# Performance work log

Measured on AMD Instinct MI355X. Metric: run time of the kernel, lower is better.

The kernel has to match this reference:

```python
import jax, jax.numpy as jnp
import numpy as np

B, S, D = 4, 2048, 768
H = 12
DH = D // H
FF = 4 * D
EPS = 1e-5


def _layernorm(x, g, b):
    mu = jnp.mean(x, axis=-1, keepdims=True)
    var = jnp.mean(jnp.square(x - mu), axis=-1, keepdims=True)
    return (x - mu) * jax.lax.rsqrt(var + EPS) * g + b


def setup_inputs() -> dict:
    key = jax.random.key(0)
    ks = jax.random.split(key, 16)
    s_d = 1.0 / np.sqrt(D)
    s_ff = 1.0 / np.sqrt(FF)
    inp = {
        "x": jax.random.normal(ks[0], (B, S, D), jnp.float32),
        # LayerNorm 1
        "ln1_g": jnp.ones((D,), jnp.float32),
        "ln1_b": jnp.zeros((D,), jnp.float32),
        # attention linears (stored as [in, out], i.e. already transposed)
        "Wq": jax.random.normal(ks[1], (D, D), jnp.float32) * s_d,
        "bq": jax.random.normal(ks[2], (D,), jnp.float32) * s_d,
        "Wk": jax.random.normal(ks[3], (D, D), jnp.float32) * s_d,
        "bk": jax.random.normal(ks[4], (D,), jnp.float32) * s_d,
        "Wv": jax.random.normal(ks[5], (D, D), jnp.float32) * s_d,
        "bv": jax.random.normal(ks[6], (D,), jnp.float32) * s_d,
        "Wo": jax.random.normal(ks[7], (D, D), jnp.float32) * s_d,
        "bo": jax.random.normal(ks[8], (D,), jnp.float32) * s_d,
        # LayerNorm 2
        "ln2_g": jnp.ones((D,), jnp.float32),
        "ln2_b": jnp.zeros((D,), jnp.float32),
        # feed-forward (bias always on, per torch code)
        "W1": jax.random.normal(ks[9], (D, FF), jnp.float32) * s_d,
        "b1": jax.random.normal(ks[10], (FF,), jnp.float32) * s_d,
        "W2": jax.random.normal(ks[11], (FF, D), jnp.float32) * s_ff,
        "b2": jax.random.normal(ks[12], (D,), jnp.float32) * s_ff,
    }
    return inp


def reference(x, ln1_g, ln1_b, Wq, bq, Wk, bk, Wv, bv, Wo, bo,
              ln2_g, ln2_b, W1, b1, W2, b2):
    # --- attention branch (pre-LN) ---
    h = _layernorm(x, ln1_g, ln1_b)
    q = (h @ Wq + bq).reshape(B, S, H, DH).transpose(0, 2, 1, 3)  # [B,H,S,DH]
    k = (h @ Wk + bk).reshape(B, S, H, DH).transpose(0, 2, 1, 3)
    v = (h @ Wv + bv).reshape(B, S, H, DH).transpose(0, 2, 1, 3)
    scores = jnp.einsum("bhqd,bhkd->bhqk", q, k) / np.sqrt(DH)
    causal = jnp.tril(jnp.ones((S, S), bool))
    scores = jnp.where(causal, scores, -jnp.inf)
    attn = jax.nn.softmax(scores, axis=-1)
    out = jnp.einsum("bhqk,bhkd->bhqd", attn, v)
    out = out.transpose(0, 2, 1, 3).reshape(B, S, D)
    x = x + (out @ Wo + bo)
    # --- feed-forward branch (pre-LN, exact GELU) ---
    h2 = _layernorm(x, ln2_g, ln2_b)
    ff = jax.nn.gelu(h2 @ W1 + b1, approximate=False) @ W2 + b2
    return x + ff
```

## Files before the change

kernel.cpp:

```cpp
#include <hip/hip_runtime.h>
#include <math.h>

#define B_ 4
#define S_ 2048
#define D_ 768
#define H_ 12
#define DH_ 64
#define FF_ 3072
#define LDQ (3*D_)

using short8  = __attribute__((ext_vector_type(8))) short;
using f32x4   = __attribute__((ext_vector_type(4))) float;
using f32x16  = __attribute__((ext_vector_type(16))) float;
using float4v = __attribute__((ext_vector_type(4))) float;
using ushort4v= __attribute__((ext_vector_type(4))) unsigned short;

__device__ __forceinline__ unsigned short f2bf(float f) {
  unsigned u = __builtin_bit_cast(unsigned, f);
  u += 0x7FFFu + ((u >> 16) & 1u);
  return (unsigned short)(u >> 16);
}

__device__ __forceinline__ unsigned cvt_pk_bf16(float a, float b) {
  unsigned r;
  asm("v_cvt_pk_bf16_f32 %0, %1, %2" : "=v"(r) : "v"(a), "v"(b));
  return r;
}

__device__ __forceinline__ void gload16(const void* g, void* l) {
  __builtin_amdgcn_global_load_lds(
      (const __attribute__((address_space(1))) unsigned*)g,
      (__attribute__((address_space(3))) unsigned*)l, 16, 0, 0);
}

__global__ __launch_bounds__(256) void transpose_cast_multi_kernel(
    const float* __restrict__ Wq, const float* __restrict__ Wk,
    const float* __restrict__ Wv, const float* __restrict__ Wo,
    const float* __restrict__ W1, const float* __restrict__ W2,
    unsigned short* __restrict__ WqT, unsigned short* __restrict__ WkT,
    unsigned short* __restrict__ WvT, unsigned short* __restrict__ WoT,
    unsigned short* __restrict__ W1T, unsigned short* __restrict__ W2T) {
  __shared__ float tile[32][33];
  int bid = blockIdx.x;
  const float* in; unsigned short* out; int K, N, t;
  if (bid < 2304) {
    int seg = bid / 576; t = bid % 576; K = D_; N = D_;
    in  = seg == 0 ? Wq  : seg == 1 ? Wk  : seg == 2 ? Wv  : Wo;
    out = seg == 0 ? WqT : seg == 1 ? WkT : seg == 2 ? WvT : WoT;
  } else if (bid < 4608) {
    t = bid - 2304; K = D_; N = FF_; in = W1; out = W1T;
  } else {
    t = bid - 4608; K = FF_; N = D_; in = W2; out = W2T;
  }
  int ntk = K / 32;
  int k0 = (t % ntk) * 32, n0 = (t / ntk) * 32;
  int tx = threadIdx.x, ty = threadIdx.y;
#pragma unroll
  for (int i = 0; i < 4; i++)
    tile[ty + 8*i][tx] = in[(size_t)(k0 + ty + 8*i) * N + n0 + tx];
  __syncthreads();
#pragma unroll
  for (int i = 0; i < 4; i++)
    out[(size_t)(n0 + ty + 8*i) * K + k0 + tx] = f2bf(tile[tx][ty + 8*i]);
}

__global__ void bias_cat_kernel(const float* __restrict__ bq, const float* __restrict__ bk,
                                const float* __restrict__ bv, float* __restrict__ dst) {
  int i = blockIdx.x * 256 + threadIdx.x;
  if (i >= 3 * D_) return;
  float v;
  if (i < D_)            v = bq[i];
  else if (i < 2 * D_)   v = bk[i - D_];
  else                   v = bv[i - 2 * D_];
  dst[i] = v;
}

__global__ __launch_bounds__(256) void layernorm_kernel(
    const float* __restrict__ x, const float* __restrict__ g,
    const float* __restrict__ b, unsigned short* __restrict__ out) {
  int wave = threadIdx.x >> 6, lane = threadIdx.x & 63;
  int row = blockIdx.x * 4 + wave;
  const float* xr = x + (size_t)row * D_;
  float4v v[3];
  float sum = 0.f, sq = 0.f;
#pragma unroll
  for (int i = 0; i < 3; i++) {
    v[i] = reinterpret_cast<const float4v*>(xr)[lane + 64*i];
#pragma unroll
    for (int j = 0; j < 4; j++) { sum += v[i][j]; sq += v[i][j]*v[i][j]; }
  }
#pragma unroll
  for (int d = 1; d < 64; d <<= 1) { sum += __shfl_xor(sum, d); sq += __shfl_xor(sq, d); }
  float mu   = sum * (1.0f / D_);
  float var  = sq  * (1.0f / D_) - mu * mu;
  float rstd = rsqrtf(var + 1e-5f);
  unsigned short* orow = out + (size_t)row * D_;
#pragma unroll
  for (int i = 0; i < 3; i++) {
    int idx = (lane + 64*i) * 4;
    ushort4v o;
#pragma unroll
    for (int j = 0; j < 4; j++)
      o[j] = f2bf((v[i][j] - mu) * rstd * g[idx + j] + b[idx + j]);
    *reinterpret_cast<ushort4v*>(orow + idx) = o;
  }
}

#define EPI_QKV   0
#define EPI_OPROJ 1
#define EPI_GELU  2
#define EPI_FINAL 3

template<int EPI>
__global__ __launch_bounds__(256) void gemm_kernel(
    const unsigned short* __restrict__ A, int lda,
    const unsigned short* __restrict__ BT, int K,
    const float* __restrict__ bias,
    const float* __restrict__ resid,
    float* __restrict__ outf,
    unsigned short* __restrict__ outh,
    int ldo, float ascale, int nN) {
  __shared__ __attribute__((aligned(16))) unsigned short Ls[3][128*64];
  int tid = threadIdx.x;
  int wave = tid >> 6, lane = tid & 63;
  int lrow = lane & 15, lk = lane >> 4;
  int bid = blockIdx.x;
  int xcd = bid & 7, j = bid >> 3;
  int nM8 = gridDim.x / (8 * nN);
  int m0 = (xcd * nM8 + j / nN) * 128;
  int n0 = (j % nN) * 128;
  int wm = (wave >> 1) * 64, wn = (wave & 1) * 64;

  auto STAGE = [&](int buf, int k0) {
#pragma unroll
    for (int i = 0; i < 4; i++) {
      int ch = i * 256 + tid;
      int row = ch >> 3, s8 = ch & 7;
      int m = s8 ^ (row & 7);
      const unsigned short* src = (m < 4)
        ? A  + (size_t)(m0 + row) * lda + k0 + m * 8
        : BT + (size_t)(n0 + row) * K   + k0 + (m - 4) * 8;
      gload16(src, &Ls[buf][(i*256 + wave*64) * 8]);
    }
  };

  f32x4 acc[4][4] = {};
  int nt = K / 32;
  STAGE(0, 0);
  STAGE(1, 32);
  for (int t = 0; t < nt; t++) {
    if (t + 1 < nt) { asm volatile("s_waitcnt vmcnt(4)" ::: "memory"); }
    else            { asm volatile("s_waitcnt vmcnt(0)" ::: "memory"); }
    __builtin_amdgcn_s_barrier();
    const unsigned short* Lc = Ls[t % 3];
    short8 af[4], bf[4];
#pragma unroll
    for (int mi = 0; mi < 4; mi++) {
      int row = wm + mi*16 + lrow;
      af[mi] = *reinterpret_cast<const short8*>(&Lc[row*64 + ((lk ^ (row & 7)) * 8)]);
    }
#pragma unroll
    for (int ni = 0; ni < 4; ni++) {
      int row = wn + ni*16 + lrow;
      bf[ni] = *reinterpret_cast<const short8*>(&Lc[row*64 + (((4 + lk) ^ (row & 7)) * 8)]);
    }
    if (t + 2 < nt) STAGE((t + 2) % 3, (t + 2) * 32);
    __builtin_amdgcn_s_setprio(1);
#pragma unroll
    for (int mi = 0; mi < 4; mi++)
#pragma unroll
      for (int ni = 0; ni < 4; ni++)
        acc[mi][ni] = __builtin_amdgcn_mfma_f32_16x16x32_bf16(af[mi], bf[ni], acc[mi][ni], 0, 0, 0);
    __builtin_amdgcn_s_setprio(0);
  }
#pragma unroll
  for (int mi = 0; mi < 4; mi++) {
#pragma unroll
    for (int ni = 0; ni < 4; ni++) {
#pragma unroll
      for (int r = 0; r < 4; r++) {
        int gm = m0 + wm + mi*16 + (lane >> 4)*4 + r;
        int gn = n0 + wn + ni*16 + lrow;
        float v = acc[mi][ni][r] + bias[gn];
        if constexpr (EPI == EPI_QKV) {
          if (gn < D_) v *= ascale;
          outh[(size_t)gm * ldo + gn] = f2bf(v);
        } else if constexpr (EPI == EPI_OPROJ) {
          size_t idx = (size_t)gm * ldo + gn;
          outf[idx] = v + resid[idx];
        } else if constexpr (EPI == EPI_GELU) {
          float gv = 0.5f * v * (1.0f + erff(v * 0.70710678118654752f));
          outh[(size_t)gm * ldo + gn] = f2bf(gv);
        } else {
          size_t idx = (size_t)gm * ldo + gn;
          outf[idx] = v + resid[idx];
        }
      }
    }
  }
}

__global__ __launch_bounds__(256, 3) void attn_kernel(
    const unsigned short* __restrict__ qkv,
    unsigned short* __restrict__ o) {
  __shared__ __attribute__((aligned(16))) unsigned short Ks[2][64*64];
  __shared__ __attribute__((aligned(16))) unsigned short VT[2][64*64];
  int tid = threadIdx.x;
  int wave = tid >> 6, lane = tid & 63;
  int ql = lane & 31, hi = lane >> 5;
  int bid = blockIdx.x;
  int xcd = bid & 7, r = bid >> 3;
  int bh = xcd * 6 + (r % 6);
  int qtile = 15 - (r / 6);
  int bb = bh / H_, hh = bh % H_;
  const unsigned short* qb = qkv + (size_t)bb * S_ * LDQ + hh * DH_;
  const unsigned short* kb = qb + D_;
  const unsigned short* vb = qb + 2 * D_;

  int sr = tid >> 2;
  int sc16 = (tid & 3) * 16;
  int kp = tid & 31, dh0 = (tid >> 5) * 8;
  uint4 krA, krB, vrA, vrB;

  auto LOADR = [&](int kb0) {
    const unsigned short* ksrc = kb + (size_t)(kb0 + sr) * LDQ + sc16;
    krA = *reinterpret_cast<const uint4*>(ksrc);
    krB = *reinterpret_cast<const uint4*>(ksrc + 8);
    const unsigned short* vsrc = vb + (size_t)(kb0 + 2*kp) * LDQ + dh0;
    vrA = *reinterpret_cast<const uint4*>(vsrc);
    vrB = *reinterpret_cast<const uint4*>(vsrc + LDQ);
  };
  auto WRITE = [&](int buf) {
    int sw = (sr & 7) << 4;
    int cb = sc16 * 2;
    *reinterpret_cast<uint4*>(&Ks[buf][(sr*128 + (cb ^ sw)) >> 1]) = krA;
    *reinterpret_cast<uint4*>(&Ks[buf][(sr*128 + ((cb + 16) ^ sw)) >> 1]) = krB;
    union { uint4 u4; unsigned short s[8]; } a, b;
    a.u4 = vrA; b.u4 = vrB;
#pragma unroll
    for (int j2 = 0; j2 < 8; j2++) {
      int row = dh0 + j2, sw2 = (row & 7) << 4;
      *reinterpret_cast<unsigned*>(&VT[buf][(row*128 + ((4*kp) ^ sw2)) >> 1]) =
          (unsigned)a.s[j2] | ((unsigned)b.s[j2] << 16);
    }
  };

  int q0 = qtile * 128;
  int qw = q0 + wave * 32;
  int myq = qw + ql;

  short8 qf[4];
#pragma unroll
  for (int dblk = 0; dblk < 4; dblk++)
    qf[dblk] = *reinterpret_cast<const short8*>(qb + (size_t)myq * LDQ + dblk*16 + hi*8);

  f32x16 oaccT[2] = {};
  float mst = -1e30f, lst = 0.f;
  int nt = q0 / 64 + 2;

  auto TILE = [&](int kt, int cur) {
    int kb0 = kt * 64;
    bool has_next = (kt + 1 < nt);
    if (has_next) LOADR((kt + 1) * 64);

    if (kb0 <= qw + 31) {
      f32x16 sc[2] = {};
      __builtin_amdgcn_s_setprio(1);
#pragma unroll
      for (int dblk = 0; dblk < 4; dblk++) {
#pragma unroll
        for (int blk = 0; blk < 2; blk++) {
          int row = blk*32 + ql;
          int sw = (row & 7) << 4;
          short8 kf = *reinterpret_cast<const short8*>(
              &Ks[cur][(row*128 + (((unsigned)(dblk*32 + hi*16)) ^ sw)) >> 1]);
          sc[blk] = __builtin_amdgcn_mfma_f32_32x32x16_bf16(kf, qf[dblk], sc[blk], 0, 0, 0);
        }
      }
      __builtin_amdgcn_s_setprio(0);
      bool full = (kb0 + 63 <= qw);
      if (!full) {
#pragma unroll
        for (int blk = 0; blk < 2; blk++)
#pragma unroll
          for (int r2 = 0; r2 < 16; r2++) {
            int key = kb0 + blk*32 + (r2 & 3) + 8*(r2 >> 2) + 4*hi;
            if (key > myq) sc[blk][r2] = -1e30f;
          }
      }
      float pm0 = -1e30f, pm1 = -1e30f, pm2 = -1e30f, pm3 = -1e30f;
#pragma unroll
      for (int blk = 0; blk < 2; blk++)
#pragma unroll
        for (int g = 0; g < 4; g++) {
          pm0 = fmaxf(pm0, sc[blk][4*g]);
          pm1 = fmaxf(pm1, sc[blk][4*g+1]);
          pm2 = fmaxf(pm2, sc[blk][4*g+2]);
          pm3 = fmaxf(pm3, sc[blk][4*g+3]);
        }
      float mx = fmaxf(fmaxf(pm0, pm1), fmaxf(pm2, pm3));
      mx = fmaxf(mx, __shfl_xor(mx, 32));
      if (!__all(mx <= mst + 8.0f)) {
        float mnew = fmaxf(mst, mx);
        float fac = exp2f(mst - mnew);
        lst *= fac;
#pragma unroll
        for (int db = 0; db < 2; db++)
#pragma unroll
          for (int r2 = 0; r2 < 16; r2++) oaccT[db][r2] *= fac;
        mst = mnew;
      }
      short8 pa[4];
      float rs = 0.f;
#pragma unroll
      for (int b = 0; b < 2; b++) {
#pragma unroll
        for (int so = 0; so < 2; so++) {
          float p0 = exp2f(sc[b][8*so + 0] - mst);
          float p1 = exp2f(sc[b][8*so + 1] - mst);
          float p2 = exp2f(sc[b][8*so + 2] - mst);
          float p3 = exp2f(sc[b][8*so + 3] - mst);
          float p4 = exp2f(sc[b][8*so + 4] - mst);
          float p5 = exp2f(sc[b][8*so + 5] - mst);
          float p6 = exp2f(sc[b][8*so + 6] - mst);
          float p7 = exp2f(sc[b][8*so + 7] - mst);
          rs += ((p0 + p1) + (p2 + p3)) + ((p4 + p5) + (p6 + p7));
          unsigned W0 = cvt_pk_bf16(p0, p1);
          unsigned W1 = cvt_pk_bf16(p2, p3);
          unsigned W2 = cvt_pk_bf16(p4, p5);
          unsigned W3 = cvt_pk_bf16(p6, p7);
          asm volatile("v_permlane32_swap_b32 %0, %1" : "+v"(W0), "+v"(W2));
          asm volatile("v_permlane32_swap_b32 %0, %1" : "+v"(W1), "+v"(W3));
          union { uint4 u; short8 s; } cvtu;
          cvtu.u.x = W0; cvtu.u.y = W1; cvtu.u.z = W2; cvtu.u.w = W3;
          pa[2*b + so] = cvtu.s;
        }
      }
      rs += __shfl_xor(rs, 32);
      lst += rs;
      __builtin_amdgcn_s_setprio(1);
#pragma unroll
      for (int ks = 0; ks < 4; ks++) {
        int cb = ks*32 + hi*16;
#pragma unroll
        for (int db = 0; db < 2; db++) {
          int row = db*32 + ql;
          int sw = (row & 7) << 4;
          short8 vf = *reinterpret_cast<const short8*>(&VT[cur][(row*128 + (cb ^ sw)) >> 1]);
          oaccT[db] = __builtin_amdgcn_mfma_f32_32x32x16_bf16(vf, pa[ks], oaccT[db], 0, 0, 0);
        }
      }
      __builtin_amdgcn_s_setprio(0);
    }

    if (has_next) WRITE(cur ^ 1);
    __syncthreads();
  };

  LOADR(0);
  WRITE(0);
  __syncthreads();
  for (int kt = 0; kt < nt; kt += 2) {
    TILE(kt, 0);
    TILE(kt + 1, 1);
  }

  float inv = 1.0f / lst;
  unsigned short* ob = o + ((size_t)(bb * S_ + myq)) * D_ + hh * DH_;
#pragma unroll
  for (int db = 0; db < 2; db++)
#pragma unroll
    for (int g = 0; g < 8; g++) {
      int r2 = 2 * g;
      int dh = db*32 + (r2 & 3) + 8*(r2 >> 2) + 4*hi;
      unsigned pk = cvt_pk_bf16(oaccT[db][r2] * inv, oaccT[db][r2+1] * inv);
      *reinterpret_cast<unsigned*>(ob + dh) = pk;
    }
}

extern "C" void kernel_launch(void* const* d_in, const int* in_sizes, int n_in,
                              void* d_out, int out_size, void* d_ws, size_t ws_size,
                              hipStream_t stream) {
  (void)in_sizes; (void)n_in; (void)out_size; (void)ws_size;
  const float* x    = (const float*)d_in[0];
  const float* ln1g = (const float*)d_in[1];
  const float* ln1b = (const float*)d_in[2];
  const float* Wq   = (const float*)d_in[3];
  const float* bq   = (const float*)d_in[4];
  const float* Wk   = (const float*)d_in[5];
  const float* bk   = (const float*)d_in[6];
  const float* Wv   = (const float*)d_in[7];
  const float* bv   = (const float*)d_in[8];
  const float* Wo   = (const float*)d_in[9];
  const float* bo   = (const float*)d_in[10];
  const float* ln2g = (const float*)d_in[11];
  const float* ln2b = (const float*)d_in[12];
  const float* W1   = (const float*)d_in[13];
  const float* b1   = (const float*)d_in[14];
  const float* W2   = (const float*)d_in[15];
  const float* b2   = (const float*)d_in[16];
  float* out = (float*)d_out;

  char* ws = (char*)d_ws;
  size_t off = 0;
  auto alloc = [&](size_t bytes) {
    char* p = ws + off;
    off += (bytes + 255) & ~(size_t)255;
    return p;
  };
  unsigned short* WqT = (unsigned short*)alloc((size_t)D_*D_*2);
  unsigned short* WkT = (unsigned short*)alloc((size_t)D_*D_*2);
  unsigned short* WvT = (unsigned short*)alloc((size_t)D_*D_*2);
  unsigned short* WoT = (unsigned short*)alloc((size_t)D_*D_*2);
  unsigned short* W1T = (unsigned short*)alloc((size_t)D_*FF_*2);
  unsigned short* W2T = (unsigned short*)alloc((size_t)FF_*D_*2);
  unsigned short* h   = (unsigned short*)alloc((size_t)B_*S_*D_*2);
  unsigned short* qkv = (unsigned short*)alloc((size_t)B_*S_*LDQ*2);
  unsigned short* ob  = (unsigned short*)alloc((size_t)B_*S_*D_*2);
  float* bias_cat     = (float*)alloc((size_t)3*D_*4);
  unsigned short* ffb = qkv;
  unsigned short* h2  = h;

  const float qscale = 0.125f * 1.4426950408889634f;

  dim3 tb(32, 8);
  transpose_cast_multi_kernel<<<6912, tb, 0, stream>>>(
      Wq, Wk, Wv, Wo, W1, W2, WqT, WkT, WvT, WoT, W1T, W2T);
  bias_cat_kernel<<<9, 256, 0, stream>>>(bq, bk, bv, bias_cat);

  layernorm_kernel<<<(B_*S_)/4, 256, 0, stream>>>(x, ln1g, ln1b, h);

  gemm_kernel<EPI_QKV><<<dim3(64*18), 256, 0, stream>>>(
      h, D_, WqT, D_, bias_cat, nullptr, nullptr, qkv, LDQ, qscale, 18);

  attn_kernel<<<dim3(768), 256, 0, stream>>>(qkv, ob);

  gemm_kernel<EPI_OPROJ><<<dim3(64*6), 256, 0, stream>>>(
      ob, D_, WoT, D_, bo, x, out, nullptr, D_, 1.0f, 6);

  layernorm_kernel<<<(B_*S_)/4, 256, 0, stream>>>(out, ln2g, ln2b, h2);

  gemm_kernel<EPI_GELU><<<dim3(64*24), 256, 0, stream>>>(
      h2, D_, W1T, D_, b1, nullptr, nullptr, ffb, FF_, 1.0f, 24);

  gemm_kernel<EPI_FINAL><<<dim3(64*6), 256, 0, stream>>>(
      ffb, FF_, W2T, FF_, b2, out, out, nullptr, D_, 1.0f, 6);
}
```

Before: 264.3 us.

## Enlarge GEMM tiles to 128x256 with 512 threads and 4-stage pipeline

Each GEMM block now runs 8 waves covering a 128x256 output tile instead of 4 waves covering 128x128. Operands are staged in separate A and B LDS buffers with a new swizzle that packs two rows per 64-element line, using precomputed offsets. Prefetch depth grows from 2 to 3 chunks across 4 buffers, and the grid mapping changes accordingly. This raises per-block data reuse and latency hiding, but halves the block count (fewer blocks for the small N=768 GEMMs) and uses more LDS per block.

```diff
diff --git a/kernel.cpp b/kernel.cpp
--- a/kernel.cpp
+++ b/kernel.cpp
@@ -112,7 +112,7 @@
 #define EPI_FINAL 3
 
 template<int EPI>
-__global__ __launch_bounds__(256) void gemm_kernel(
+__global__ __launch_bounds__(512) void gemm_kernel(
     const unsigned short* __restrict__ A, int lda,
     const unsigned short* __restrict__ BT, int K,
     const float* __restrict__ bias,
@@ -120,66 +120,87 @@
     float* __restrict__ outf,
     unsigned short* __restrict__ outh,
     int ldo, float ascale, int nN) {
-  __shared__ __attribute__((aligned(16))) unsigned short Ls[3][128*64];
+  __shared__ __attribute__((aligned(16))) unsigned short As4[4][64*64];
+  __shared__ __attribute__((aligned(16))) unsigned short Bs4[4][128*64];
   int tid = threadIdx.x;
-  int wave = tid >> 6, lane = tid & 63;
+  int wid = tid >> 6, lane = tid & 63;
   int lrow = lane & 15, lk = lane >> 4;
   int bid = blockIdx.x;
   int xcd = bid & 7, j = bid >> 3;
-  int nM8 = gridDim.x / (8 * nN);
-  int m0 = (xcd * nM8 + j / nN) * 128;
-  int n0 = (j % nN) * 128;
-  int wm = (wave >> 1) * 64, wn = (wave & 1) * 64;
-
-  auto STAGE = [&](int buf, int k0) {
-#pragma unroll
-    for (int i = 0; i < 4; i++) {
-      int ch = i * 256 + tid;
-      int row = ch >> 3, s8 = ch & 7;
-      int m = s8 ^ (row & 7);
-      const unsigned short* src = (m < 4)
-        ? A  + (size_t)(m0 + row) * lda + k0 + m * 8
-        : BT + (size_t)(n0 + row) * K   + k0 + (m - 4) * 8;
-      gload16(src, &Ls[buf][(i*256 + wave*64) * 8]);
-    }
+  int m0 = (xcd * 8 + (j & 7)) * 128;
+  int n0 = (j >> 3) * 256;
+  int wm = (wid >> 2) * 64;
+  int wn = (wid & 3) * 64;
+
+  int urA = tid >> 3, s8A = tid & 7, mA = s8A ^ (urA & 7);
+  const unsigned short* srcA = A + (size_t)(m0 + 2*urA + (mA >> 2)) * lda + (mA & 3) * 8;
+  int urB0 = tid >> 3, mB0 = (tid & 7) ^ (urB0 & 7);
+  const unsigned short* srcB0 = BT + (size_t)(n0 + 2*urB0 + (mB0 >> 2)) * K + (mB0 & 3) * 8;
+  int ch1 = 512 + tid;
+  int urB1 = ch1 >> 3, mB1 = (ch1 & 7) ^ (urB1 & 7);
+  const unsigned short* srcB1 = BT + (size_t)(n0 + 2*urB1 + (mB1 >> 2)) * K + (mB1 & 3) * 8;
+  int wbase = wid * 512;
+
+  int offA[4], offB[4];
+#pragma unroll
+  for (int mi = 0; mi < 4; mi++) {
+    int ar = wm + mi*16 + lrow;
+    int ur = ar >> 1;
+    int s = (((ar & 1) << 2) | lk) ^ (ur & 7);
+    offA[mi] = ur * 64 + s * 8;
+  }
+#pragma unroll
+  for (int ni = 0; ni < 4; ni++) {
+    int br = wn + ni*16 + lrow;
+    int ur = br >> 1;
+    int s = (((br & 1) << 2) | lk) ^ (ur & 7);
+    offB[ni] = ur * 64 + s * 8;
+  }
+
+  auto STAGE = [&](int slot, int c) {
+    const unsigned short* sa = srcA + c * 32;
+    const unsigned short* s0 = srcB0 + c * 32;
+    const unsigned short* s1 = srcB1 + c * 32;
+    gload16(sa, &As4[slot][wbase]);
+    gload16(s0, &Bs4[slot][wbase]);
+    gload16(s1, &Bs4[slot][4096 + wbase]);
   };
 
   f32x4 acc[4][4] = {};
-  int nt = K / 32;
-  STAGE(0, 0);
-  STAGE(1, 32);
-  for (int t = 0; t < nt; t++) {
-    if (t + 1 < nt) { asm volatile("s_waitcnt vmcnt(4)" ::: "memory"); }
-    else            { asm volatile("s_waitcnt vmcnt(0)" ::: "memory"); }
+  int nc = K / 32;
+  STAGE(0, 0); STAGE(1, 1); STAGE(2, 2);
+  for (int c = 0; c < nc; c++) {
+    if (c + 2 < nc)      { asm volatile("s_waitcnt vmcnt(6)" ::: "memory"); }
+    else if (c + 1 < nc) { asm volatile("s_waitcnt vmcnt(3)" ::: "memory"); }
+    else                 { asm volatile("s_waitcnt vmcnt(0)" ::: "memory"); }
     __builtin_amdgcn_s_barrier();
-    const unsigned short* Lc = Ls[t % 3];
-    short8 af[4], bf[4];
-#pragma unroll
-    for (int mi = 0; mi < 4; mi++) {
-      int row = wm + mi*16 + lrow;
-      af[mi] = *reinterpret_cast<const short8*>(&Lc[row*64 + ((lk ^ (row & 7)) * 8)]);
-    }
+    int slot = c & 3;
+    const unsigned short* Ac = As4[slot];
+    const unsigned short* Bc = Bs4[slot];
+    short8 a_[4], b_[4];
+#pragma unroll
+    for (int ni = 0; ni < 4; ni++)
+      b_[ni] = *reinterpret_cast<const short8*>(&Bc[offB[ni]]);
+#pragma unroll
+    for (int mi = 0; mi < 4; mi++)
+      a_[mi] = *reinterpret_cast<const short8*>(&Ac[offA[mi]]);
+    if (c + 3 < nc) STAGE((c + 3) & 3, c + 3);
+    __builtin_amdgcn_s_setprio(1);
+#pragma unroll
+    for (int mi = 0; mi < 4; mi++)
+#pragma unroll
+      for (int ni = 0; ni < 4; ni++)
+        acc[mi][ni] = __builtin_amdgcn_mfma_f32_16x16x32_bf16(a_[mi], b_[ni], acc[mi][ni], 0, 0, 0);
+    __builtin_amdgcn_s_setprio(0);
+  }
+
+#pragma unroll
+  for (int mi = 0; mi < 4; mi++) {
 #pragma unroll
     for (int ni = 0; ni < 4; ni++) {
-      int row = wn + ni*16 + lrow;
-      bf[ni] = *reinterpret_cast<const short8*>(&Lc[row*64 + (((4 + lk) ^ (row & 7)) * 8)]);
-    }
-    if (t + 2 < nt) STAGE((t + 2) % 3, (t + 2) * 32);
-    __builtin_amdgcn_s_setprio(1);
-#pragma unroll
-    for (int mi = 0; mi < 4; mi++)
-#pragma unroll
-      for (int ni = 0; ni < 4; ni++)
-        acc[mi][ni] = __builtin_amdgcn_mfma_f32_16x16x32_bf16(af[mi], bf[ni], acc[mi][ni], 0, 0, 0);
-    __builtin_amdgcn_s_setprio(0);
-  }
-#pragma unroll
-  for (int mi = 0; mi < 4; mi++) {
-#pragma unroll
-    for (int ni = 0; ni < 4; ni++) {
 #pragma unroll
       for (int r = 0; r < 4; r++) {
-        int gm = m0 + wm + mi*16 + (lane >> 4)*4 + r;
+        int gm = m0 + wm + mi*16 + lk*4 + r;
         int gn = n0 + wn + ni*16 + lrow;
         float v = acc[mi][ni][r] + bias[gn];
         if constexpr (EPI == EPI_QKV) {
@@ -430,19 +451,19 @@
 
   layernorm_kernel<<<(B_*S_)/4, 256, 0, stream>>>(x, ln1g, ln1b, h);
 
-  gemm_kernel<EPI_QKV><<<dim3(64*18), 256, 0, stream>>>(
-      h, D_, WqT, D_, bias_cat, nullptr, nullptr, qkv, LDQ, qscale, 18);
+  gemm_kernel<EPI_QKV><<<dim3(8*8*9), 512, 0, stream>>>(
+      h, D_, WqT, D_, bias_cat, nullptr, nullptr, qkv, LDQ, qscale, 9);
 
   attn_kernel<<<dim3(768), 256, 0, stream>>>(qkv, ob);
 
-  gemm_kernel<EPI_OPROJ><<<dim3(64*6), 256, 0, stream>>>(
-      ob, D_, WoT, D_, bo, x, out, nullptr, D_, 1.0f, 6);
+  gemm_kernel<EPI_OPROJ><<<dim3(8*8*3), 512, 0, stream>>>(
+      ob, D_, WoT, D_, bo, x, out, nullptr, D_, 1.0f, 3);
 
   layernorm_kernel<<<(B_*S_)/4, 256, 0, stream>>>(out, ln2g, ln2b, h2);
 
-  gemm_kernel<EPI_GELU><<<dim3(64*24), 256, 0, stream>>>(
-      h2, D_, W1T, D_, b1, nullptr, nullptr, ffb, FF_, 1.0f, 24);
-
-  gemm_kernel<EPI_FINAL><<<dim3(64*6), 256, 0, stream>>>(
-      ffb, FF_, W2T, FF_, b2, out, out, nullptr, D_, 1.0f, 6);
-}
+  gemm_kernel<EPI_GELU><<<dim3(8*8*12), 512, 0, stream>>>(
+      h2, D_, W1T, D_, b1, nullptr, nullptr, ffb, FF_, 1.0f, 12);
+
+  gemm_kernel<EPI_FINAL><<<dim3(8*8*3), 512, 0, stream>>>(
+      ffb, FF_, W2T, FF_, b2, out, out, nullptr, D_, 1.0f, 3);
+}
```

New measurement: 284.9 us. 7.8% more time.
